# Kernel optimization log

Measured on AMD Instinct MI355X. Metric: run time of the kernel, lower is better.

## Reference

```python
import jax, jax.numpy as jnp
import numpy as np

# rp = [l1, l2] link parameters (stand-in for the repo's robot-parameter object)
RP = jnp.array([1.0, 1.0], dtype=jnp.float32)
EPS = 1e-8


def _mlp(x, w1, b1, w2, b2, w3, b3):
    # Linear(2,16) -> Softplus -> Linear(16,16) -> Softplus -> Linear(16,2)
    h = jax.nn.softplus(x @ w1.T + b1)
    h = jax.nn.softplus(h @ w2.T + b2)
    return h @ w3.T + b3


def _analytic_theta_0(qi):
    # smooth analytic coordinate (stand-in for transforms.analytic_theta_0)
    return RP[0] * jnp.arctan2(qi[1], qi[0])


def _analytic_theta_1(qi):
    return RP[1] * jnp.sqrt(qi[0] ** 2 + qi[1] ** 2 + EPS)


def setup_inputs() -> dict:
    key = jax.random.key(0)
    ks = jax.random.split(key, 13)
    N = 1_000_000
    q = jax.random.normal(ks[0], (N, 2), dtype=jnp.float32)

    def lin(k, out_d, in_d):
        kw, kb = jax.random.split(k)
        s = 1.0 / np.sqrt(in_d)
        w = jax.random.uniform(kw, (out_d, in_d), jnp.float32, -s, s)
        b = jax.random.uniform(kb, (out_d,), jnp.float32, -s, s)
        return w, b

    enc_w1, enc_b1 = lin(ks[1], 16, 2)
    enc_w2, enc_b2 = lin(ks[2], 16, 16)
    enc_w3, enc_b3 = lin(ks[3], 2, 16)
    dec_w1, dec_b1 = lin(ks[4], 16, 2)
    dec_w2, dec_b2 = lin(ks[5], 16, 16)
    dec_w3, dec_b3 = lin(ks[6], 2, 16)
    return dict(q=q,
                enc_w1=enc_w1, enc_b1=enc_b1, enc_w2=enc_w2, enc_b2=enc_b2,
                enc_w3=enc_w3, enc_b3=enc_b3,
                dec_w1=dec_w1, dec_b1=dec_b1, dec_w2=dec_w2, dec_b2=dec_b2,
                dec_w3=dec_w3, dec_b3=dec_b3)


def reference(q, enc_w1, enc_b1, enc_w2, enc_b2, enc_w3, enc_b3,
              dec_w1, dec_b1, dec_w2, dec_b2, dec_w3, dec_b3):
    enc = lambda x: _mlp(x, enc_w1, enc_b1, enc_w2, enc_b2, enc_w3, enc_b3)
    dec = lambda x: _mlp(x, dec_w1, dec_b1, dec_w2, dec_b2, dec_w3, dec_b3)

    # analytic jacobians (per-sample fn returns shape (1,) like unsqueeze(0))
    def f0(qi):
        t = jnp.expand_dims(_analytic_theta_0(qi), 0)
        return t, t

    def f1(qi):
        t = jnp.expand_dims(_analytic_theta_1(qi), 0)
        return t, t

    J0, _ = jax.vmap(jax.jacfwd(f0, has_aux=True))(q)  # [N,1,2]
    J1, _ = jax.vmap(jax.jacfwd(f1, has_aux=True))(q)  # [N,1,2]
    J_h_ana = jnp.concatenate([J0, J1], axis=1).astype(jnp.float32)  # [N,2,2]

    theta = enc(q)                                  # [N,2]
    J_h = jax.vmap(jax.jacfwd(enc))(q)              # [N,2,2]
    q_hat = dec(theta)                              # [N,2]
    J_h_dec = jax.vmap(jax.jacfwd(dec))(theta)      # [N,2,2]
    return theta, J_h, q_hat, J_h_dec, J_h_ana
```

## Files before the change

kernel.cpp:

```cpp
#include <hip/hip_runtime.h>
#include <math.h>


typedef float  f32x16 __attribute__((ext_vector_type(16)));
typedef short  bf16x8 __attribute__((ext_vector_type(8)));

__device__ __forceinline__ unsigned short f2bf1(float f) {
    unsigned u = __builtin_bit_cast(unsigned, f);
    u += 0x7FFFu + ((u >> 16) & 1u);
    return (unsigned short)(u >> 16);
}

__device__ __forceinline__ unsigned packbf(float a, float b) {
    return __builtin_amdgcn_perm(__builtin_bit_cast(unsigned, b),
                                 __builtin_bit_cast(unsigned, a), 0x07060302u);
}

__device__ __forceinline__ bf16x8 pack8(const float* v) {
    union { unsigned u[4]; bf16x8 f; } x;
    x.u[0] = packbf(v[0], v[1]); x.u[1] = packbf(v[2], v[3]);
    x.u[2] = packbf(v[4], v[5]); x.u[3] = packbf(v[6], v[7]);
    return x.f;
}

__device__ __forceinline__ void activ(float z, float& sp, float& sg) {
    float t = __expf(-z);
    sg = __builtin_amdgcn_rcpf(1.0f + t);
    sp = fmaf(-0.69314718056f, __log2f(sg), z);
}

__device__ __forceinline__ bf16x8 b3frag(const float* v, int h) {
    unsigned P01 = packbf(v[0], v[1]), P23 = packbf(v[2], v[3]);
    unsigned P45 = packbf(v[4], v[5]), P67 = packbf(v[6], v[7]);
    unsigned S0 = h ? P01 : P45;
    unsigned S1 = h ? P23 : P67;
    unsigned R0 = (unsigned)__shfl_xor((int)S0, 32);
    unsigned R1 = (unsigned)__shfl_xor((int)S1, 32);
    union { unsigned u[4]; bf16x8 f; } x;
    x.u[0] = h ? R0 : P01; x.u[1] = h ? R1 : P23;
    x.u[2] = h ? P45 : R0; x.u[3] = h ? P67 : R1;
    return x.f;
}

__global__ void prep_kernel(
    const float* __restrict__ ew1, const float* __restrict__ eb1,
    const float* __restrict__ ew2, const float* __restrict__ eb2,
    const float* __restrict__ ew3,
    const float* __restrict__ dw1, const float* __restrict__ db1,
    const float* __restrict__ dw2, const float* __restrict__ db2,
    const float* __restrict__ dw3,
    float* __restrict__ ws)
{
    const int t = threadIdx.x;
    if (t >= 64) return;
    const int h = t >> 5, m = t & 31;
    unsigned short* frag = (unsigned short*)(ws + 4096);
#pragma unroll
    for (int jj = 0; jj < 8; ++jj) {
        const int j = 8 * h + jj;
        ws[t*24 + jj]             = ew1[2*j];
        ws[t*24 + 8 + jj]         = ew1[2*j + 1];
        ws[t*24 + 16 + jj]        = eb1[j];
        ws[1536 + t*24 + jj]      = dw1[2*j];
        ws[1536 + t*24 + 8 + jj]  = dw1[2*j + 1];
        ws[1536 + t*24 + 16 + jj] = db1[j];
        frag[t*8 + jj]        = (m < 16) ? f2bf1(ew2[m*16 + j]) : (unsigned short)0;
        frag[1024 + t*8 + jj] = (m < 16) ? f2bf1(dw2[m*16 + j]) : (unsigned short)0;
        float a3e = 0.0f, a3d = 0.0f;
        if (m < 2)                 { a3e = ew3[m*16 + j];      a3d = dw3[m*16 + j]; }
        else if (m == 4 || m == 5) { a3e = ew3[(m-4)*16 + j];  a3d = dw3[(m-4)*16 + j]; }
        frag[512 + t*8 + jj]  = f2bf1(a3e);
        frag[1536 + t*8 + jj] = f2bf1(a3d);
    }
#pragma unroll
    for (int r = 0; r < 8; ++r) {
        const int i = (r & 3) + 8 * (r >> 2) + 4 * h;
        ws[3072 + t*8 + r] = eb2[i];
        ws[3584 + t*8 + r] = db2[i];
    }
}

__device__ __forceinline__ void mlp_mfma(
    const float* __restrict__ L1, const float* __restrict__ B2,
    bf16x8 A2, bf16x8 A3, float b30, float b31,
    float x0, float x1, int h,
    float& o0, float& o1, float& J00, float& J01, float& J10, float& J11)
{
    float h1[8], ta[8], tb[8];
#pragma unroll
    for (int jj = 0; jj < 8; ++jj) {
        float wa = L1[jj], wb = L1[8 + jj], bb = L1[16 + jj];
        float z = fmaf(wa, x0, fmaf(wb, x1, bb));
        float sp, sg; activ(z, sp, sg);
        h1[jj] = sp; ta[jj] = sg * wa; tb[jj] = sg * wb;
    }
    bf16x8 Bh = pack8(h1), Bta = pack8(ta), Btb = pack8(tb);
    f32x16 zc, ua, ub;
#pragma unroll
    for (int r = 0; r < 8; ++r) { zc[r] = B2[r]; ua[r] = 0.0f; ub[r] = 0.0f; }
    zc = __builtin_amdgcn_mfma_f32_32x32x16_bf16(A2, Bh,  zc, 0, 0, 0);
    ua = __builtin_amdgcn_mfma_f32_32x32x16_bf16(A2, Bta, ua, 0, 0, 0);
    ub = __builtin_amdgcn_mfma_f32_32x32x16_bf16(A2, Btb, ub, 0, 0, 0);

    float h2[8], sa[8], sb[8];
#pragma unroll
    for (int r = 0; r < 8; ++r) {
        float z = zc[r];
        float sp, sg; activ(z, sp, sg);
        h2[r] = sp; sa[r] = sg * ua[r]; sb[r] = sg * ub[r];
    }
    bf16x8 B3h = b3frag(h2, h), B3a = b3frag(sa, h), B3b = b3frag(sb, h);
    f32x16 oz, oa, ob;
    oz[0] = b30; oz[1] = b31;
    oa[0] = 0.0f; oa[1] = 0.0f;
    ob[0] = 0.0f; ob[1] = 0.0f;
    oz = __builtin_amdgcn_mfma_f32_32x32x16_bf16(A3, B3h, oz, 0, 0, 0);
    oa = __builtin_amdgcn_mfma_f32_32x32x16_bf16(A3, B3a, oa, 0, 0, 0);
    ob = __builtin_amdgcn_mfma_f32_32x32x16_bf16(A3, B3b, ob, 0, 0, 0);
    o0 = oz[0]; o1 = oz[1];
    J00 = oa[0]; J10 = oa[1]; J01 = ob[0]; J11 = ob[1];
}

__device__ __forceinline__ void do_group(
    const float* __restrict__ q, float* __restrict__ out, int n, int sbase,
    int s32, int h,
    const float* __restrict__ encL1, const float* __restrict__ decL1,
    const float* __restrict__ encB2, const float* __restrict__ decB2,
    bf16x8 A2e, bf16x8 A3e, bf16x8 A2d, bf16x8 A3d,
    float eb30, float eb31, float db30, float db31)
{
    const int sample = sbase + s32;
    const int sidx = sample < n ? sample : n - 1;

    const float2 qv = ((const float2*)q)[sidx];
    const float x = qv.x, y = qv.y;

    float eo0, eo1, eJ00, eJ01, eJ10, eJ11;
    mlp_mfma(encL1, encB2, A2e, A3e, eb30, eb31, x, y, h,
             eo0, eo1, eJ00, eJ01, eJ10, eJ11);

    const float tx = eo0, ty = eo1;

    float qo0, qo1, dJ00, dJ01, dJ10, dJ11;
    mlp_mfma(decL1, decB2, A2d, A3d, db30, db31, tx, ty, h,
             qo0, qo1, dJ00, dJ01, dJ10, dJ11);

    if (h == 0 && sample < n) {
        const float r2   = fmaf(x, x, y * y);
        const float iv   = __builtin_amdgcn_rcpf(r2);
        const float rinv = __builtin_amdgcn_rsqf(r2 + 1e-8f);
        const size_t nn = (size_t)n;
        ((float2*)(out))[sample]           = make_float2(eo0, eo1);
        ((float4*)(out + 2 * nn))[sample]  = make_float4(eJ00, eJ01, eJ10, eJ11);
        ((float2*)(out + 6 * nn))[sample]  = make_float2(qo0, qo1);
        ((float4*)(out + 8 * nn))[sample]  = make_float4(dJ00, dJ01, dJ10, dJ11);
        ((float4*)(out + 12 * nn))[sample] = make_float4(-y * iv, x * iv, x * rinv, y * rinv);
    }
}

__global__ __launch_bounds__(256) void ae_mfma_kernel(
    const float* __restrict__ q,
    const float* __restrict__ eb3, const float* __restrict__ db3,
    const float* __restrict__ ws, float* __restrict__ out, int n)
{
    const int lane = threadIdx.x & 63;
    const int w = blockIdx.x * 4 + (threadIdx.x >> 6);
    const int s32 = lane & 31, h = lane >> 5;
    const long base = (long)w * 64;
    if (base >= n) return;

    const float* encL1 = ws + (size_t)lane * 24;
    const float* decL1 = ws + 1536 + (size_t)lane * 24;
    const float* encB2 = ws + 3072 + (size_t)lane * 8;
    const float* decB2 = ws + 3584 + (size_t)lane * 8;
    const bf16x8* fr = (const bf16x8*)(ws + 4096);
    const bf16x8 A2e = fr[lane], A3e = fr[64 + lane];
    const bf16x8 A2d = fr[128 + lane], A3d = fr[192 + lane];
    const float eb30 = eb3[0], eb31 = eb3[1];
    const float db30 = db3[0], db31 = db3[1];

    do_group(q, out, n, (int)base, s32, h, encL1, decL1, encB2, decB2,
             A2e, A3e, A2d, A3d, eb30, eb31, db30, db31);
    if (base + 32 < n)
        do_group(q, out, n, (int)base + 32, s32, h, encL1, decL1, encB2, decB2,
                 A2e, A3e, A2d, A3d, eb30, eb31, db30, db31);
}

extern "C" void kernel_launch(void* const* d_in, const int* in_sizes, int n_in,
                              void* d_out, int out_size, void* d_ws, size_t ws_size,
                              hipStream_t stream)
{
    const float* q   = (const float*)d_in[0];
    const float* ew1 = (const float*)d_in[1];
    const float* eb1 = (const float*)d_in[2];
    const float* ew2 = (const float*)d_in[3];
    const float* eb2 = (const float*)d_in[4];
    const float* ew3 = (const float*)d_in[5];
    const float* eb3 = (const float*)d_in[6];
    const float* dw1 = (const float*)d_in[7];
    const float* db1 = (const float*)d_in[8];
    const float* dw2 = (const float*)d_in[9];
    const float* db2 = (const float*)d_in[10];
    const float* dw3 = (const float*)d_in[11];
    const float* db3 = (const float*)d_in[12];

    const int n = in_sizes[0] / 2;
    float* ws = (float*)d_ws;

    prep_kernel<<<1, 64, 0, stream>>>(ew1, eb1, ew2, eb2, ew3,
                                      dw1, db1, dw2, db2, dw3, ws);

    const int waves  = (n + 63) / 64;
    const int blocks = (waves + 3) / 4;
    ae_mfma_kernel<<<blocks, 256, 0, stream>>>(q, eb3, db3, ws, (float*)d_out, n);
}
```

Before: 137.4 us.

## Switch MLP layers to 16x16x16 bf16 MFMA with 16-sample column groups

Replaces the 32x32x16 MFMA scheme, which padded the 16-wide hidden layer to 32 rows and handled 32 samples per group, with 16x16x16 MFMAs that match the 16-wide hidden layer and process 16 samples per call, four chunks per wave. This drops the wasted half of each MFMA and the cross-half shuffles that built the layer-3 operand. All 64 lanes now store outputs, picking their sample's values with selects, where before only half the lanes stored. The cost is more MFMA calls per wave, more activation work per lane and more live registers.

```diff
diff --git a/kernel.cpp b/kernel.cpp
--- a/kernel.cpp
+++ b/kernel.cpp
@@ -2,8 +2,8 @@
 #include <math.h>
 
 
-typedef float  f32x16 __attribute__((ext_vector_type(16)));
-typedef short  bf16x8 __attribute__((ext_vector_type(8)));
+typedef float  f32x4  __attribute__((ext_vector_type(4)));
+typedef short  bf16x4 __attribute__((ext_vector_type(4)));
 
 __device__ __forceinline__ unsigned short f2bf1(float f) {
     unsigned u = __builtin_bit_cast(unsigned, f);
@@ -16,30 +16,27 @@
                                  __builtin_bit_cast(unsigned, a), 0x07060302u);
 }
 
-__device__ __forceinline__ bf16x8 pack8(const float* v) {
-    union { unsigned u[4]; bf16x8 f; } x;
-    x.u[0] = packbf(v[0], v[1]); x.u[1] = packbf(v[2], v[3]);
-    x.u[2] = packbf(v[4], v[5]); x.u[3] = packbf(v[6], v[7]);
+__device__ __forceinline__ bf16x4 pack4(float a, float b, float c, float d) {
+    union { unsigned u[2]; bf16x4 f; } x;
+    x.u[0] = packbf(a, b); x.u[1] = packbf(c, d);
     return x.f;
+}
+
+__device__ __forceinline__ f32x4 mfma16(bf16x4 a, bf16x4 b, f32x4 c) {
+#if __has_builtin(__builtin_amdgcn_mfma_f32_16x16x16bf16_1k)
+    return __builtin_amdgcn_mfma_f32_16x16x16bf16_1k(a, b, c, 0, 0, 0);
+#else
+    f32x4 d;
+    asm("v_mfma_f32_16x16x16_bf16 %0, %1, %2, %3"
+        : "=&v"(d) : "v"(a), "v"(b), "v"(c));
+    return d;
+#endif
 }
 
 __device__ __forceinline__ void activ(float z, float& sp, float& sg) {
     float t = __expf(-z);
     sg = __builtin_amdgcn_rcpf(1.0f + t);
     sp = fmaf(-0.69314718056f, __log2f(sg), z);
-}
-
-__device__ __forceinline__ bf16x8 b3frag(const float* v, int h) {
-    unsigned P01 = packbf(v[0], v[1]), P23 = packbf(v[2], v[3]);
-    unsigned P45 = packbf(v[4], v[5]), P67 = packbf(v[6], v[7]);
-    unsigned S0 = h ? P01 : P45;
-    unsigned S1 = h ? P23 : P67;
-    unsigned R0 = (unsigned)__shfl_xor((int)S0, 32);
-    unsigned R1 = (unsigned)__shfl_xor((int)S1, 32);
-    union { unsigned u[4]; bf16x8 f; } x;
-    x.u[0] = h ? R0 : P01; x.u[1] = h ? R1 : P23;
-    x.u[2] = h ? P45 : R0; x.u[3] = h ? P67 : R1;
-    return x.f;
 }
 
 __global__ void prep_kernel(
@@ -53,137 +50,124 @@
 {
     const int t = threadIdx.x;
     if (t >= 64) return;
-    const int h = t >> 5, m = t & 31;
-    unsigned short* frag = (unsigned short*)(ws + 4096);
-#pragma unroll
-    for (int jj = 0; jj < 8; ++jj) {
-        const int j = 8 * h + jj;
-        ws[t*24 + jj]             = ew1[2*j];
-        ws[t*24 + 8 + jj]         = ew1[2*j + 1];
-        ws[t*24 + 16 + jj]        = eb1[j];
-        ws[1536 + t*24 + jj]      = dw1[2*j];
-        ws[1536 + t*24 + 8 + jj]  = dw1[2*j + 1];
-        ws[1536 + t*24 + 16 + jj] = db1[j];
-        frag[t*8 + jj]        = (m < 16) ? f2bf1(ew2[m*16 + j]) : (unsigned short)0;
-        frag[1024 + t*8 + jj] = (m < 16) ? f2bf1(dw2[m*16 + j]) : (unsigned short)0;
-        float a3e = 0.0f, a3d = 0.0f;
-        if (m < 2)                 { a3e = ew3[m*16 + j];      a3d = dw3[m*16 + j]; }
-        else if (m == 4 || m == 5) { a3e = ew3[(m-4)*16 + j];  a3d = dw3[(m-4)*16 + j]; }
-        frag[512 + t*8 + jj]  = f2bf1(a3e);
-        frag[1536 + t*8 + jj] = f2bf1(a3d);
-    }
-#pragma unroll
-    for (int r = 0; r < 8; ++r) {
-        const int i = (r & 3) + 8 * (r >> 2) + 4 * h;
-        ws[3072 + t*8 + r] = eb2[i];
-        ws[3584 + t*8 + r] = db2[i];
-    }
-}
-
-__device__ __forceinline__ void mlp_mfma(
-    const float* __restrict__ L1, const float* __restrict__ B2,
-    bf16x8 A2, bf16x8 A3, float b30, float b31,
-    float x0, float x1, int h,
+    const int g = t >> 4, m = t & 15;
+    unsigned short* frag = (unsigned short*)(ws + 2048);
+#pragma unroll
+    for (int j = 0; j < 4; ++j) {
+        const int i = g * 4 + j;
+        ws[t*12 + j]           = ew1[2*i];
+        ws[t*12 + 4 + j]       = ew1[2*i + 1];
+        ws[t*12 + 8 + j]       = eb1[i];
+        ws[768 + t*12 + j]     = dw1[2*i];
+        ws[768 + t*12 + 4 + j] = dw1[2*i + 1];
+        ws[768 + t*12 + 8 + j] = db1[i];
+        ws[1536 + t*4 + j]     = eb2[i];
+        ws[1792 + t*4 + j]     = db2[i];
+        frag[t*4 + j]       = f2bf1(ew2[m*16 + i]);
+        frag[512 + t*4 + j] = f2bf1(dw2[m*16 + i]);
+        const int r3 = m & 3;
+        frag[256 + t*4 + j] = (r3 < 2) ? f2bf1(ew3[r3*16 + i]) : (unsigned short)0;
+        frag[768 + t*4 + j] = (r3 < 2) ? f2bf1(dw3[r3*16 + i]) : (unsigned short)0;
+    }
+}
+
+__device__ __forceinline__ void mlp16(
+    f32x4 Wa, f32x4 Wb, f32x4 Bb, f32x4 B2c,
+    bf16x4 A2, bf16x4 A3, f32x4 C3, f32x4 Z,
+    float x, float y,
     float& o0, float& o1, float& J00, float& J01, float& J10, float& J11)
 {
-    float h1[8], ta[8], tb[8];
-#pragma unroll
-    for (int jj = 0; jj < 8; ++jj) {
-        float wa = L1[jj], wb = L1[8 + jj], bb = L1[16 + jj];
-        float z = fmaf(wa, x0, fmaf(wb, x1, bb));
+    float h[4], ta[4], tb[4];
+#pragma unroll
+    for (int j = 0; j < 4; ++j) {
+        float z = fmaf(Wa[j], x, fmaf(Wb[j], y, Bb[j]));
         float sp, sg; activ(z, sp, sg);
-        h1[jj] = sp; ta[jj] = sg * wa; tb[jj] = sg * wb;
-    }
-    bf16x8 Bh = pack8(h1), Bta = pack8(ta), Btb = pack8(tb);
-    f32x16 zc, ua, ub;
-#pragma unroll
-    for (int r = 0; r < 8; ++r) { zc[r] = B2[r]; ua[r] = 0.0f; ub[r] = 0.0f; }
-    zc = __builtin_amdgcn_mfma_f32_32x32x16_bf16(A2, Bh,  zc, 0, 0, 0);
-    ua = __builtin_amdgcn_mfma_f32_32x32x16_bf16(A2, Bta, ua, 0, 0, 0);
-    ub = __builtin_amdgcn_mfma_f32_32x32x16_bf16(A2, Btb, ub, 0, 0, 0);
-
-    float h2[8], sa[8], sb[8];
-#pragma unroll
-    for (int r = 0; r < 8; ++r) {
-        float z = zc[r];
-        float sp, sg; activ(z, sp, sg);
+        h[j] = sp; ta[j] = sg * Wa[j]; tb[j] = sg * Wb[j];
+    }
+    f32x4 zc = mfma16(A2, pack4(h[0],  h[1],  h[2],  h[3]),  B2c);
+    f32x4 ua = mfma16(A2, pack4(ta[0], ta[1], ta[2], ta[3]), Z);
+    f32x4 ub = mfma16(A2, pack4(tb[0], tb[1], tb[2], tb[3]), Z);
+
+    float h2[4], sa[4], sb[4];
+#pragma unroll
+    for (int r = 0; r < 4; ++r) {
+        float sp, sg; activ(zc[r], sp, sg);
         h2[r] = sp; sa[r] = sg * ua[r]; sb[r] = sg * ub[r];
     }
-    bf16x8 B3h = b3frag(h2, h), B3a = b3frag(sa, h), B3b = b3frag(sb, h);
-    f32x16 oz, oa, ob;
-    oz[0] = b30; oz[1] = b31;
-    oa[0] = 0.0f; oa[1] = 0.0f;
-    ob[0] = 0.0f; ob[1] = 0.0f;
-    oz = __builtin_amdgcn_mfma_f32_32x32x16_bf16(A3, B3h, oz, 0, 0, 0);
-    oa = __builtin_amdgcn_mfma_f32_32x32x16_bf16(A3, B3a, oa, 0, 0, 0);
-    ob = __builtin_amdgcn_mfma_f32_32x32x16_bf16(A3, B3b, ob, 0, 0, 0);
+    f32x4 oz = mfma16(A3, pack4(h2[0], h2[1], h2[2], h2[3]), C3);
+    f32x4 oa = mfma16(A3, pack4(sa[0], sa[1], sa[2], sa[3]), Z);
+    f32x4 ob = mfma16(A3, pack4(sb[0], sb[1], sb[2], sb[3]), Z);
     o0 = oz[0]; o1 = oz[1];
     J00 = oa[0]; J10 = oa[1]; J01 = ob[0]; J11 = ob[1];
 }
 
-__device__ __forceinline__ void do_group(
-    const float* __restrict__ q, float* __restrict__ out, int n, int sbase,
-    int s32, int h,
-    const float* __restrict__ encL1, const float* __restrict__ decL1,
-    const float* __restrict__ encB2, const float* __restrict__ decB2,
-    bf16x8 A2e, bf16x8 A3e, bf16x8 A2d, bf16x8 A3d,
-    float eb30, float eb31, float db30, float db31)
-{
-    const int sample = sbase + s32;
-    const int sidx = sample < n ? sample : n - 1;
-
-    const float2 qv = ((const float2*)q)[sidx];
-    const float x = qv.x, y = qv.y;
-
-    float eo0, eo1, eJ00, eJ01, eJ10, eJ11;
-    mlp_mfma(encL1, encB2, A2e, A3e, eb30, eb31, x, y, h,
-             eo0, eo1, eJ00, eJ01, eJ10, eJ11);
-
-    const float tx = eo0, ty = eo1;
-
-    float qo0, qo1, dJ00, dJ01, dJ10, dJ11;
-    mlp_mfma(decL1, decB2, A2d, A3d, db30, db31, tx, ty, h,
-             qo0, qo1, dJ00, dJ01, dJ10, dJ11);
-
-    if (h == 0 && sample < n) {
+__device__ __forceinline__ float sel4(const float* v, int g) {
+    float a = (g & 1) ? v[1] : v[0];
+    float b = (g & 1) ? v[3] : v[2];
+    return (g & 2) ? b : a;
+}
+
+__global__ __launch_bounds__(256) void ae_mfma_kernel(
+    const float* __restrict__ q,
+    const float* __restrict__ eb3, const float* __restrict__ db3,
+    const float* __restrict__ ws, float* __restrict__ out, int n)
+{
+    const int lane = threadIdx.x & 63;
+    const int wv = blockIdx.x * 4 + (threadIdx.x >> 6);
+    const int g = lane >> 4, m16 = lane & 15;
+    const long base = (long)wv * 64;
+    if (base >= n) return;
+
+    const f32x4 eWa = *(const f32x4*)(ws + (size_t)lane*12);
+    const f32x4 eWb = *(const f32x4*)(ws + (size_t)lane*12 + 4);
+    const f32x4 eBb = *(const f32x4*)(ws + (size_t)lane*12 + 8);
+    const f32x4 dWa = *(const f32x4*)(ws + 768 + (size_t)lane*12);
+    const f32x4 dWb = *(const f32x4*)(ws + 768 + (size_t)lane*12 + 4);
+    const f32x4 dBb = *(const f32x4*)(ws + 768 + (size_t)lane*12 + 8);
+    const f32x4 eB2 = *(const f32x4*)(ws + 1536 + (size_t)lane*4);
+    const f32x4 dB2 = *(const f32x4*)(ws + 1792 + (size_t)lane*4);
+    const bf16x4* fr = (const bf16x4*)(ws + 2048);
+    const bf16x4 A2e = fr[lane],       A3e = fr[64 + lane];
+    const bf16x4 A2d = fr[128 + lane], A3d = fr[192 + lane];
+    f32x4 C3e; C3e[0] = eb3[0]; C3e[1] = eb3[1]; C3e[2] = 0.0f; C3e[3] = 0.0f;
+    f32x4 C3d; C3d[0] = db3[0]; C3d[1] = db3[1]; C3d[2] = 0.0f; C3d[3] = 0.0f;
+    f32x4 Z;   Z[0] = 0.0f; Z[1] = 0.0f; Z[2] = 0.0f; Z[3] = 0.0f;
+
+    float xs[4], ys[4];
+#pragma unroll
+    for (int c = 0; c < 4; ++c) {
+        long s = base + c*16 + m16;
+        long si = s < n ? s : (long)n - 1;
+        const float2 qv = ((const float2*)q)[si];
+        xs[c] = qv.x; ys[c] = qv.y;
+    }
+
+    float eo0[4], eo1[4], E00[4], E01[4], E10[4], E11[4];
+    float qo0[4], qo1[4], D00[4], D01[4], D10[4], D11[4];
+#pragma unroll
+    for (int c = 0; c < 4; ++c) {
+        mlp16(eWa, eWb, eBb, eB2, A2e, A3e, C3e, Z, xs[c], ys[c],
+              eo0[c], eo1[c], E00[c], E01[c], E10[c], E11[c]);
+        mlp16(dWa, dWb, dBb, dB2, A2d, A3d, C3d, Z, eo0[c], eo1[c],
+              qo0[c], qo1[c], D00[c], D01[c], D10[c], D11[c]);
+    }
+
+    const long sp = base + lane;
+    if (sp < n) {
+        const float x = sel4(xs, g), y = sel4(ys, g);
         const float r2   = fmaf(x, x, y * y);
         const float iv   = __builtin_amdgcn_rcpf(r2);
         const float rinv = __builtin_amdgcn_rsqf(r2 + 1e-8f);
         const size_t nn = (size_t)n;
-        ((float2*)(out))[sample]           = make_float2(eo0, eo1);
-        ((float4*)(out + 2 * nn))[sample]  = make_float4(eJ00, eJ01, eJ10, eJ11);
-        ((float2*)(out + 6 * nn))[sample]  = make_float2(qo0, qo1);
-        ((float4*)(out + 8 * nn))[sample]  = make_float4(dJ00, dJ01, dJ10, dJ11);
-        ((float4*)(out + 12 * nn))[sample] = make_float4(-y * iv, x * iv, x * rinv, y * rinv);
-    }
-}
-
-__global__ __launch_bounds__(256) void ae_mfma_kernel(
-    const float* __restrict__ q,
-    const float* __restrict__ eb3, const float* __restrict__ db3,
-    const float* __restrict__ ws, float* __restrict__ out, int n)
-{
-    const int lane = threadIdx.x & 63;
-    const int w = blockIdx.x * 4 + (threadIdx.x >> 6);
-    const int s32 = lane & 31, h = lane >> 5;
-    const long base = (long)w * 64;
-    if (base >= n) return;
-
-    const float* encL1 = ws + (size_t)lane * 24;
-    const float* decL1 = ws + 1536 + (size_t)lane * 24;
-    const float* encB2 = ws + 3072 + (size_t)lane * 8;
-    const float* decB2 = ws + 3584 + (size_t)lane * 8;
-    const bf16x8* fr = (const bf16x8*)(ws + 4096);
-    const bf16x8 A2e = fr[lane], A3e = fr[64 + lane];
-    const bf16x8 A2d = fr[128 + lane], A3d = fr[192 + lane];
-    const float eb30 = eb3[0], eb31 = eb3[1];
-    const float db30 = db3[0], db31 = db3[1];
-
-    do_group(q, out, n, (int)base, s32, h, encL1, decL1, encB2, decB2,
-             A2e, A3e, A2d, A3d, eb30, eb31, db30, db31);
-    if (base + 32 < n)
-        do_group(q, out, n, (int)base + 32, s32, h, encL1, decL1, encB2, decB2,
-                 A2e, A3e, A2d, A3d, eb30, eb31, db30, db31);
+        ((float2*)(out))[sp]           = make_float2(sel4(eo0,g), sel4(eo1,g));
+        ((float4*)(out + 2 * nn))[sp]  = make_float4(sel4(E00,g), sel4(E01,g),
+                                                     sel4(E10,g), sel4(E11,g));
+        ((float2*)(out + 6 * nn))[sp]  = make_float2(sel4(qo0,g), sel4(qo1,g));
+        ((float4*)(out + 8 * nn))[sp]  = make_float4(sel4(D00,g), sel4(D01,g),
+                                                     sel4(D10,g), sel4(D11,g));
+        ((float4*)(out + 12 * nn))[sp] = make_float4(-y * iv, x * iv,
+                                                     x * rinv, y * rinv);
+    }
 }
 
 extern "C" void kernel_launch(void* const* d_in, const int* in_sizes, int n_in,
```

New measurement: 167.8 us. 22.1% more time.
